# Kernel tuning notes

Hardware: AMD Instinct MI355X
Metric: run time of the kernel (lower is better)

Reference implementation:

```python
import jax, jax.numpy as jnp
import numpy as np

H = 32  # node_hidden_size
B = 16  # number of graphs in the batch


def setup_inputs() -> dict:
    key = jax.random.key(0)
    ks = iter(jax.random.split(key, 32))
    N, E = 20000, 200000
    rn = lambda s, scale=0.1: jax.random.normal(next(ks), s, dtype=jnp.float32) * scale
    return {
        "x": jax.random.normal(next(ks), (N, 4), dtype=jnp.float32),
        "edge_index": jax.random.randint(next(ks), (2, E), 0, N),
        "edge_attr": jax.random.normal(next(ks), (E,), dtype=jnp.float32),
        "batch": jnp.sort(jax.random.randint(next(ks), (N,), 0, B)),
        # project: Linear(4,32)
        "proj_w": rn((4, H)), "proj_b": jnp.zeros((H,), jnp.float32),
        # edge_nn: Linear(1,8) -> ReLU -> Linear(8,32*32)
        "e1_w": rn((1, 8)), "e1_b": jnp.zeros((8,), jnp.float32),
        "e2_w": rn((8, H * H)), "e2_b": jnp.zeros((H * H,), jnp.float32),
        # NNConv root weight + bias
        "root_w": rn((H, H)), "conv_b": jnp.zeros((H,), jnp.float32),
        # GRU(32,32), torch layout [3H, in]/[3H, H], gate order r,z,n
        "gru_wi": rn((3 * H, H)), "gru_wh": rn((3 * H, H)),
        "gru_bi": jnp.zeros((3 * H,), jnp.float32), "gru_bh": jnp.zeros((3 * H,), jnp.float32),
        # Set2Set LSTM(2H -> H), gate order i,f,g,o
        "lstm_wi": rn((4 * H, 2 * H)), "lstm_wh": rn((4 * H, H)),
        "lstm_bi": jnp.zeros((4 * H,), jnp.float32), "lstm_bh": jnp.zeros((4 * H,), jnp.float32),
        # FFN: 2H -> H -> H -> 1 (dropout is identity at inference)
        "f1_w": rn((2 * H, H)), "f1_b": jnp.zeros((H,), jnp.float32),
        "f2_w": rn((H, H)), "f2_b": jnp.zeros((H,), jnp.float32),
        "f3_w": rn((H, 1)), "f3_b": jnp.zeros((1,), jnp.float32),
    }


def reference(x, edge_index, edge_attr, batch,
              proj_w, proj_b, e1_w, e1_b, e2_w, e2_b, root_w, conv_b,
              gru_wi, gru_wh, gru_bi, gru_bh,
              lstm_wi, lstm_wh, lstm_bi, lstm_bh,
              f1_w, f1_b, f2_w, f2_b, f3_w, f3_b):
    N = x.shape[0]
    src, dst = edge_index[0], edge_index[1]

    # project node features
    h = jax.nn.relu(x @ proj_w + proj_b)              # [N, H]
    msg = h                                           # GRU hidden state

    # edge-conditioned weights (edge_attr unsqueezed to [E,1]); constant over steps
    ea = edge_attr[:, None]
    ew = (jax.nn.relu(ea @ e1_w + e1_b) @ e2_w + e2_b).reshape(-1, H, H)  # [E, in, out]

    for _ in range(3):  # message passing steps
        m = jnp.einsum('ei,eio->eo', h[src], ew)                  # per-edge matvec [E, H]
        agg = jax.ops.segment_sum(m, dst, num_segments=N)         # scatter-add to targets
        out = jax.nn.relu(agg + h @ root_w + conv_b)              # NNConv root + bias, then ReLU
        # GRU cell (seq_len=1)
        gi = out @ gru_wi.T + gru_bi
        gh = msg @ gru_wh.T + gru_bh
        r = jax.nn.sigmoid(gi[:, :H] + gh[:, :H])
        z = jax.nn.sigmoid(gi[:, H:2 * H] + gh[:, H:2 * H])
        n = jnp.tanh(gi[:, 2 * H:] + r * gh[:, 2 * H:])
        h = (1.0 - z) * n + z * msg
        msg = h

    # Set2Set readout, processing_steps=1
    q_star = jnp.zeros((B, 2 * H), x.dtype)
    hL = jnp.zeros((B, H), x.dtype)
    cL = jnp.zeros((B, H), x.dtype)
    g = q_star @ lstm_wi.T + lstm_bi + hL @ lstm_wh.T + lstm_bh   # [B, 4H]
    i_g = jax.nn.sigmoid(g[:, :H])
    f_g = jax.nn.sigmoid(g[:, H:2 * H])
    g_g = jnp.tanh(g[:, 2 * H:3 * H])
    o_g = jax.nn.sigmoid(g[:, 3 * H:])
    cL = f_g * cL + i_g * g_g
    q = o_g * jnp.tanh(cL)                                        # [B, H]
    # per-graph softmax attention
    e = jnp.sum(h * q[batch], axis=-1)                            # [N]
    e_max = jax.ops.segment_max(e, batch, num_segments=B)
    a = jnp.exp(e - e_max[batch])
    a = a / jax.ops.segment_sum(a, batch, num_segments=B)[batch]
    r_out = jax.ops.segment_sum(a[:, None] * h, batch, num_segments=B)  # [B, H]
    q_star = jnp.concatenate([q, r_out], axis=-1)                 # [B, 2H]

    # FFN (dropout = identity at inference)
    out = jax.nn.relu(q_star @ f1_w + f1_b)
    out = jax.nn.relu(out @ f2_w + f2_b)
    return out @ f3_w + f3_b                                      # [B, 1]
```

## Files before the change

### kernel.cpp

```cpp
#include <hip/hip_runtime.h>
#include <math.h>

#define H 32
#define BSEG 16
#define CHUNKS 32

#define FMA4(acc, s, wv) { acc[0]=fmaf(s,wv.x,acc[0]); acc[1]=fmaf(s,wv.y,acc[1]); acc[2]=fmaf(s,wv.z,acc[2]); acc[3]=fmaf(s,wv.w,acc[3]); }

__device__ __forceinline__ float sigmoidf_(float x){ return 1.f/(1.f+expf(-x)); }

__device__ __forceinline__ unsigned int fenc(float f) {
    int i = __float_as_int(f);
    return (i >= 0) ? ((unsigned int)i | 0x80000000u) : ~(unsigned int)i;
}
__device__ __forceinline__ float fdec(unsigned int u) {
    int i = (u & 0x80000000u) ? (int)(u & 0x7FFFFFFFu) : (int)(~u);
    return __int_as_float(i);
}

__global__ __launch_bounds__(512) void k_prep(
    const float* __restrict__ gru_wi, const float* __restrict__ gru_wh,
    const float* __restrict__ gru_bi, const float* __restrict__ gru_bh,
    const float* __restrict__ lstm_bi, const float* __restrict__ lstm_bh,
    const float* __restrict__ e1w, const float* __restrict__ e1b, const float* __restrict__ e2w,
    float* __restrict__ WI, float* __restrict__ WH, float* __restrict__ BS,
    float* __restrict__ MP, float* __restrict__ MM, int* __restrict__ flag,
    float* __restrict__ qvec, unsigned int* __restrict__ segmax,
    float* __restrict__ ssum, float* __restrict__ vsum,
    int* __restrict__ cnt, int N)
{
    int t = threadIdx.x;
    for (int i = t; i < N; i += 512) cnt[i] = 0;
    for (int idx = t; idx < 3072; idx += 512) {
        int k = idx >> 10, rem = idx & 1023, i = rem >> 5, o = rem & 31;
        WI[idx] = gru_wi[(k*32 + o)*32 + i];
        WH[idx] = gru_wh[(k*32 + o)*32 + i];
    }
    for (int idx = t; idx < 1024; idx += 512) {
        float mp = 0.f, mm = 0.f;
        #pragma unroll
        for (int k = 0; k < 8; ++k) {
            float w = e1w[k];
            float v = e2w[k*1024 + idx];
            if (w > 0.f) mp = fmaf(w, v, mp);
            if (w < 0.f) mm = fmaf(w, v, mm);
        }
        MP[idx] = mp;
        MM[idx] = mm;
    }
    if (t == 0) {
        int z = 1;
        for (int k = 0; k < 8; ++k) if (e1b[k] != 0.f) z = 0;
        flag[0] = z;
    }
    if (t < 32) {
        BS[t]      = gru_bi[t]      + gru_bh[t];
        BS[32 + t] = gru_bi[32 + t] + gru_bh[32 + t];
        BS[64 + t] = gru_bi[64 + t];
        BS[96 + t] = gru_bh[64 + t];
    }
    if (t < H) {
        float g0 = lstm_bi[t] + lstm_bh[t];
        float g2 = lstm_bi[2*H + t] + lstm_bh[2*H + t];
        float g3 = lstm_bi[3*H + t] + lstm_bh[3*H + t];
        float ig = sigmoidf_(g0);
        float gg = tanhf(g2);
        float og = sigmoidf_(g3);
        qvec[t] = og * tanhf(ig * gg);
    }
    for (int i = t; i < BSEG; i += 512) { segmax[i] = 0u; ssum[i] = 0.f; }
    for (int i = t; i < BSEG*H; i += 512) vsum[i] = 0.f;
}

__global__ __launch_bounds__(256) void k_count(const int* __restrict__ ei, int* __restrict__ cnt, int E)
{
    int e = blockIdx.x * 256 + threadIdx.x;
    if (e < E) atomicAdd(&cnt[ei[E + e]], 1);
}

__global__ __launch_bounds__(1024) void k_scan(
    const int* __restrict__ cnt, int* __restrict__ rowptr, int* __restrict__ cursor, int N)
{
    __shared__ int part[1024];
    int t = threadIdx.x;
    int chunk = (N + 1023) >> 10;
    int base = t * chunk;
    int s = 0;
    for (int i = 0; i < chunk; ++i) {
        int idx = base + i;
        if (idx < N) s += cnt[idx];
    }
    part[t] = s;
    __syncthreads();
    for (int off = 1; off < 1024; off <<= 1) {
        int add = (t >= off) ? part[t - off] : 0;
        __syncthreads();
        part[t] += add;
        __syncthreads();
    }
    int run = part[t] - s;
    for (int i = 0; i < chunk; ++i) {
        int idx = base + i;
        if (idx < N) {
            rowptr[idx] = run;
            cursor[idx] = run;
            run += cnt[idx];
        }
    }
    if (t == 1023) rowptr[N] = part[1023];
}

__global__ __launch_bounds__(256) void k_scatter(
    const int* __restrict__ ei, const float* __restrict__ ea, int* __restrict__ cursor,
    int* __restrict__ esrc, float* __restrict__ eattr, int E)
{
    int e = blockIdx.x * 256 + threadIdx.x;
    if (e >= E) return;
    int dst = ei[E + e];
    int pos = atomicAdd(&cursor[dst], 1);
    esrc[pos] = ei[e];
    eattr[pos] = ea[e];
}

__device__ __forceinline__ void pass2_lds(const float* sm, int xb, int w0, int w1, int fg4,
                                          float a[4], float b[4])
{
    #pragma unroll 2
    for (int i4 = 0; i4 < 32; i4 += 4) {
        float4 xv  = *(const float4*)&sm[xb + i4];
        float4 w00 = *(const float4*)&sm[w0 + (i4+0)*32 + fg4];
        float4 w01 = *(const float4*)&sm[w0 + (i4+1)*32 + fg4];
        float4 w02 = *(const float4*)&sm[w0 + (i4+2)*32 + fg4];
        float4 w03 = *(const float4*)&sm[w0 + (i4+3)*32 + fg4];
        float4 w10 = *(const float4*)&sm[w1 + (i4+0)*32 + fg4];
        float4 w11 = *(const float4*)&sm[w1 + (i4+1)*32 + fg4];
        float4 w12 = *(const float4*)&sm[w1 + (i4+2)*32 + fg4];
        float4 w13 = *(const float4*)&sm[w1 + (i4+3)*32 + fg4];
        FMA4(a, xv.x, w00) FMA4(a, xv.y, w01) FMA4(a, xv.z, w02) FMA4(a, xv.w, w03)
        FMA4(b, xv.x, w10) FMA4(b, xv.y, w11) FMA4(b, xv.z, w12) FMA4(b, xv.w, w13)
    }
}

__device__ __forceinline__ void pass1_lds(const float* sm, int xb, int w0, int fg4, float a[4])
{
    #pragma unroll 2
    for (int i4 = 0; i4 < 32; i4 += 4) {
        float4 xv  = *(const float4*)&sm[xb + i4];
        float4 w00 = *(const float4*)&sm[w0 + (i4+0)*32 + fg4];
        float4 w01 = *(const float4*)&sm[w0 + (i4+1)*32 + fg4];
        float4 w02 = *(const float4*)&sm[w0 + (i4+2)*32 + fg4];
        float4 w03 = *(const float4*)&sm[w0 + (i4+3)*32 + fg4];
        FMA4(a, xv.x, w00) FMA4(a, xv.y, w01) FMA4(a, xv.z, w02) FMA4(a, xv.w, w03)
    }
}

#define TW 3072
__global__ __launch_bounds__(256, 2) void k_tab(
    const float* __restrict__ x, const float* __restrict__ proj_w, const float* __restrict__ proj_b,
    const float* __restrict__ e2w, const float* __restrict__ e2b,
    const float* __restrict__ MP, const float* __restrict__ MM, const int* __restrict__ flag,
    float* __restrict__ h, float* __restrict__ A, int N)
{
    __shared__ float sm[TW + 4*288];
    int tid = threadIdx.x;
    int lane = tid & 63;
    int w = tid >> 6;
    int fg = lane & 7, fg4 = fg*4;
    int nw = lane >> 3;
    int n = (blockIdx.x * 4 + w) * 8 + nw;
    bool valid = (n < N);
    int nc = valid ? n : (N - 1);
    int xb = TW + w*288 + nw*36;

    {
        float4 xv = *(const float4*)&x[nc*4];
        float r_[4];
        #pragma unroll
        for (int j = 0; j < 4; ++j) {
            int o = fg4 + j;
            float a = proj_b[o];
            a = fmaf(xv.x, proj_w[0*32 + o], a);
            a = fmaf(xv.y, proj_w[1*32 + o], a);
            a = fmaf(xv.z, proj_w[2*32 + o], a);
            a = fmaf(xv.w, proj_w[3*32 + o], a);
            r_[j] = fmaxf(a, 0.f);
        }
        if (valid) *(float4*)&h[n*32 + fg4] = make_float4(r_[0], r_[1], r_[2], r_[3]);
        *(float4*)&sm[xb + fg4] = make_float4(r_[0], r_[1], r_[2], r_[3]);
    }

    if (flag[0]) {
        float4* s4 = (float4*)sm;
        for (int i = tid; i < 768; i += 256) {
            const float4* src = (i < 256) ? (const float4*)MP
                              : (i < 512) ? (const float4*)MM
                                          : (const float4*)e2b;
            s4[i] = src[i & 255];
        }
        __syncthreads();
        #pragma unroll 1
        for (int cc = 0; cc < 3; ++cc) {
            float acc[4] = {0.f, 0.f, 0.f, 0.f};
            pass1_lds(sm, xb, cc*1024, fg4, acc);
            if (valid)
                *(float4*)&A[(size_t)n*96 + cc*32 + fg4] =
                    make_float4(acc[0], acc[1], acc[2], acc[3]);
        }
    } else {
        #pragma unroll 1
        for (int cg = 0; cg < 3; ++cg) {
            __syncthreads();
            float4* s4 = (float4*)sm;
            for (int i = tid; i < 768; i += 256) {
                int c = cg*3 + (i >> 8);
                const float4* src = (c < 8) ? (const float4*)(e2w + (size_t)c*1024)
                                            : (const float4*)e2b;
                s4[i] = src[i & 255];
            }
            __syncthreads();
            #pragma unroll 1
            for (int cc = 0; cc < 3; ++cc) {
                float acc[4] = {0.f, 0.f, 0.f, 0.f};
                pass1_lds(sm, xb, cc*1024, fg4, acc);
                if (valid)
                    *(float4*)&A[(size_t)n*288 + (cg*3+cc)*32 + fg4] =
                        make_float4(acc[0], acc[1], acc[2], acc[3]);
            }
        }
    }
}

#define XGR 10240
__global__ __launch_bounds__(256, 2) void k_gru(
    float* __restrict__ h,
    const int* __restrict__ rowptr, const int* __restrict__ esrc, const float* __restrict__ eattr,
    const float* __restrict__ TIN, const int* __restrict__ flag,
    const float* __restrict__ root_w, const float* __restrict__ conv_b,
    const float* __restrict__ WI, const float* __restrict__ WH, const float* __restrict__ BS,
    const float* __restrict__ MP, const float* __restrict__ MM,
    const float* __restrict__ e2b, const float* __restrict__ e2w,
    const float* __restrict__ e1w, const float* __restrict__ e1b,
    float* __restrict__ TOUT, int N, int computeT)
{
    __shared__ float sm[XGR + 1152];
    int tid = threadIdx.x;
    int fast = flag[0];
    {
        float4* s4 = (float4*)sm;
        const float4* r4  = (const float4*)root_w;
        const float4* wh4 = (const float4*)WH;
        const float4* wi4 = (const float4*)WI;
        for (int i = tid; i < 256; i += 256) s4[i] = r4[i];
        for (int i = tid; i < 768; i += 256) s4[256  + i] = wh4[i];
        for (int i = tid; i < 768; i += 256) s4[1024 + i] = wi4[i];
        if (computeT && fast) {
            for (int i = tid; i < 768; i += 256) {
                const float4* src = (i < 256) ? (const float4*)MP
                                  : (i < 512) ? (const float4*)MM
                                              : (const float4*)e2b;
                s4[1792 + i] = src[i & 255];
            }
        }
    }
    __syncthreads();

    int lane = tid & 63;
    int w = tid >> 6;
    int fg = lane & 7, fg4 = fg*4;
    int nw = lane >> 3;
    int n = (blockIdx.x * 4 + w) * 8 + nw;
    bool valid = (n < N);
    int nc = valid ? n : (N - 1);
    int xb = XGR + w*288 + nw*36;

    float4 hv4 = *(const float4*)&h[nc*32 + fg4];
    float hold[4] = {hv4.x, hv4.y, hv4.z, hv4.w};
    *(float4*)&sm[xb + fg4] = hv4;

    float av[4] = {0.f, 0.f, 0.f, 0.f};
    {
        int beg = rowptr[nc];
        int end = rowptr[nc + 1];
        if (fast) {
            int j = beg;
            for (; j + 3 < end; j += 4) {
                int s0 = esrc[j],     s1 = esrc[j + 1];
                int s2 = esrc[j + 2], s3 = esrc[j + 3];
                float a0 = eattr[j],     a1 = eattr[j + 1];
                float a2 = eattr[j + 2], a3 = eattr[j + 3];
                const float* p0 = TIN + (size_t)s0 * 96;
                const float* p1 = TIN + (size_t)s1 * 96;
                const float* p2 = TIN + (size_t)s2 * 96;
                const float* p3 = TIN + (size_t)s3 * 96;
                float4 q0 = *(const float4*)&p0[(a0 > 0.f ? 0 : 32) + fg4];
                float4 r0 = *(const float4*)&p0[64 + fg4];
                float4 q1 = *(const float4*)&p1[(a1 > 0.f ? 0 : 32) + fg4];
                float4 r1 = *(const float4*)&p1[64 + fg4];
                float4 q2 = *(const float4*)&p2[(a2 > 0.f ? 0 : 32) + fg4];
                float4 r2 = *(const float4*)&p2[64 + fg4];
                float4 q3 = *(const float4*)&p3[(a3 > 0.f ? 0 : 32) + fg4];
                float4 r3 = *(const float4*)&p3[64 + fg4];
                av[0] += fmaf(a0, q0.x, r0.x) + fmaf(a1, q1.x, r1.x)
                       + fmaf(a2, q2.x, r2.x) + fmaf(a3, q3.x, r3.x);
                av[1] += fmaf(a0, q0.y, r0.y) + fmaf(a1, q1.y, r1.y)
                       + fmaf(a2, q2.y, r2.y) + fmaf(a3, q3.y, r3.y);
                av[2] += fmaf(a0, q0.z, r0.z) + fmaf(a1, q1.z, r1.z)
                       + fmaf(a2, q2.z, r2.z) + fmaf(a3, q3.z, r3.z);
                av[3] += fmaf(a0, q0.w, r0.w) + fmaf(a1, q1.w, r1.w)
                       + fmaf(a2, q2.w, r2.w) + fmaf(a3, q3.w, r3.w);
            }
            for (; j < end; ++j) {
                int s0 = esrc[j];
                float a0 = eattr[j];
                const float* p0 = TIN + (size_t)s0 * 96;
                float4 q0 = *(const float4*)&p0[(a0 > 0.f ? 0 : 32) + fg4];
                float4 r0 = *(const float4*)&p0[64 + fg4];
                av[0] += fmaf(a0, q0.x, r0.x);
                av[1] += fmaf(a0, q0.y, r0.y);
                av[2] += fmaf(a0, q0.z, r0.z);
                av[3] += fmaf(a0, q0.w, r0.w);
            }
        } else {
            for (int j = beg; j < end; ++j) {
                int src = esrc[j];
                float a = eattr[j];
                const float* Gp = TIN + (size_t)src * 288;
                float4 b = *(const float4*)&Gp[256 + fg4];
                float m0 = b.x, m1 = b.y, m2 = b.z, m3 = b.w;
                #pragma unroll
                for (int k = 0; k < 8; ++k) {
                    float t = fmaxf(fmaf(a, e1w[k], e1b[k]), 0.f);
                    float4 g = *(const float4*)&Gp[k*32 + fg4];
                    m0 = fmaf(t, g.x, m0); m1 = fmaf(t, g.y, m1);
                    m2 = fmaf(t, g.z, m2); m3 = fmaf(t, g.w, m3);
                }
                av[0] += m0; av[1] += m1; av[2] += m2; av[3] += m3;
            }
        }
    }

    float outv[4], gh2[4];
    {
        float4 cb4 = *(const float4*)&conv_b[fg4];
        outv[0]=av[0]+cb4.x; outv[1]=av[1]+cb4.y; outv[2]=av[2]+cb4.z; outv[3]=av[3]+cb4.w;
        float4 b3 = *(const float4*)&BS[96 + fg4];
        gh2[0]=b3.x; gh2[1]=b3.y; gh2[2]=b3.z; gh2[3]=b3.w;
    }
    pass2_lds(sm, xb, 0, 1024 + 2048, fg4, outv, gh2);

    float gh0[4] = {0.f,0.f,0.f,0.f};
    float gh1[4] = {0.f,0.f,0.f,0.f};
    pass2_lds(sm, xb, 1024, 2048, fg4, gh0, gh1);

    float outr[4];
    #pragma unroll
    for (int j = 0; j < 4; ++j) outr[j] = fmaxf(outv[j], 0.f);

    *(float4*)&sm[xb + fg4] = make_float4(outr[0], outr[1], outr[2], outr[3]);

    float gi0[4], gi1[4], gi2[4];
    {
        float4 b0 = *(const float4*)&BS[fg4];
        float4 b1 = *(const float4*)&BS[32 + fg4];
        float4 b2 = *(const float4*)&BS[64 + fg4];
        gi0[0]=b0.x; gi0[1]=b0.y; gi0[2]=b0.z; gi0[3]=b0.w;
        gi1[0]=b1.x; gi1[1]=b1.y; gi1[2]=b1.z; gi1[3]=b1.w;
        gi2[0]=b2.x; gi2[1]=b2.y; gi2[2]=b2.z; gi2[3]=b2.w;
    }
    pass2_lds(sm, xb, 4096, 5120, fg4, gi0, gi1);
    pass1_lds(sm, xb, 6144, fg4, gi2);

    float hnew[4];
    #pragma unroll
    for (int j = 0; j < 4; ++j) {
        float r = sigmoidf_(gi0[j] + gh0[j]);
        float z = sigmoidf_(gi1[j] + gh1[j]);
        float nn = tanhf(gi2[j] + r * gh2[j]);
        hnew[j] = (1.f - z) * nn + z * hold[j];
    }
    if (valid) *(float4*)&h[n*32 + fg4] = make_float4(hnew[0], hnew[1], hnew[2], hnew[3]);

    if (computeT) {
        *(float4*)&sm[xb + fg4] = make_float4(hnew[0], hnew[1], hnew[2], hnew[3]);
        if (fast) {
            #pragma unroll 1
            for (int cc = 0; cc < 3; ++cc) {
                float acc[4] = {0.f, 0.f, 0.f, 0.f};
                pass1_lds(sm, xb, 7168 + cc*1024, fg4, acc);
                if (valid)
                    *(float4*)&TOUT[(size_t)n*96 + cc*32 + fg4] =
                        make_float4(acc[0], acc[1], acc[2], acc[3]);
            }
        } else {
            #pragma unroll 1
            for (int cg = 0; cg < 3; ++cg) {
                __syncthreads();
                float4* s4 = (float4*)sm;
                for (int i = tid; i < 768; i += 256) {
                    int c = cg*3 + (i >> 8);
                    const float4* src = (c < 8) ? (const float4*)(e2w + (size_t)c*1024)
                                                : (const float4*)e2b;
                    s4[1792 + i] = src[i & 255];
                }
                __syncthreads();
                #pragma unroll 1
                for (int cc = 0; cc < 3; ++cc) {
                    float acc[4] = {0.f, 0.f, 0.f, 0.f};
                    pass1_lds(sm, xb, 7168 + cc*1024, fg4, acc);
                    if (valid)
                        *(float4*)&TOUT[(size_t)n*288 + (cg*3+cc)*32 + fg4] =
                            make_float4(acc[0], acc[1], acc[2], acc[3]);
                }
            }
        }
    }
}

__global__ __launch_bounds__(256) void k_pass1(
    const float* __restrict__ h, const int* __restrict__ batch,
    const float* __restrict__ qvec, float* __restrict__ ebuf,
    unsigned int* __restrict__ segmax, int N)
{
    int b = blockIdx.x / CHUNKS;
    int c = blockIdx.x % CHUNKS;
    int lo = 0, hi = N;
    while (lo < hi) { int mid = (lo + hi) >> 1; if (batch[mid] < b) lo = mid + 1; else hi = mid; }
    int s = lo;
    lo = 0; hi = N;
    while (lo < hi) { int mid = (lo + hi) >> 1; if (batch[mid] < b + 1) lo = mid + 1; else hi = mid; }
    int e = lo;
    int len = e - s;
    int per = (len + CHUNKS - 1) / CHUNKS;
    int n0 = s + c * per;
    int n1 = min(n0 + per, e);

    int tid = threadIdx.x;
    int ln = tid >> 5, o = tid & 31;
    float qv = qvec[o];
    float mloc = -INFINITY;
    for (int nn = n0 + ln; nn < n1; nn += 8) {
        float v = h[nn * H + o] * qv;
        #pragma unroll
        for (int m = 16; m >= 1; m >>= 1) v += __shfl_xor(v, m);
        if (o == 0) ebuf[nn] = v;
        mloc = fmaxf(mloc, v);
    }
    __shared__ float red[256];
    red[tid] = mloc;
    __syncthreads();
    for (int st = 128; st >= 1; st >>= 1) {
        if (tid < st) red[tid] = fmaxf(red[tid], red[tid + st]);
        __syncthreads();
    }
    if (tid == 0 && n0 < n1) atomicMax(&segmax[b], fenc(red[0]));
}

__global__ __launch_bounds__(256) void k_pass2(
    const float* __restrict__ h, const int* __restrict__ batch,
    const float* __restrict__ ebuf, const unsigned int* __restrict__ segmax,
    float* __restrict__ ssum, float* __restrict__ vsum, int N)
{
    int b = blockIdx.x / CHUNKS;
    int c = blockIdx.x % CHUNKS;
    int lo = 0, hi = N;
    while (lo < hi) { int mid = (lo + hi) >> 1; if (batch[mid] < b) lo = mid + 1; else hi = mid; }
    int s = lo;
    lo = 0; hi = N;
    while (lo < hi) { int mid = (lo + hi) >> 1; if (batch[mid] < b + 1) lo = mid + 1; else hi = mid; }
    int e = lo;
    int len = e - s;
    int per = (len + CHUNKS - 1) / CHUNKS;
    int n0 = s + c * per;
    int n1 = min(n0 + per, e);

    int tid = threadIdx.x;
    int ln = tid >> 5, o = tid & 31;
    float emax = fdec(segmax[b]);
    float vacc = 0.f, sacc = 0.f;
    for (int nn = n0 + ln; nn < n1; nn += 8) {
        float a = expf(ebuf[nn] - emax);
        vacc += a * h[nn * H + o];
        if (o == 0) sacc += a;
    }
    __shared__ float vsh[8][H];
    __shared__ float ssh[8];
    vsh[ln][o] = vacc;
    if (o == 0) ssh[ln] = sacc;
    __syncthreads();
    if (tid < H) {
        float v = 0.f;
        #pragma unroll
        for (int g = 0; g < 8; ++g) v += vsh[g][tid];
        atomicAdd(&vsum[b * H + tid], v);
    } else if (tid == H) {
        float stot = 0.f;
        #pragma unroll
        for (int g = 0; g < 8; ++g) stot += ssh[g];
        atomicAdd(&ssum[b], stot);
    }
}

__global__ __launch_bounds__(512) void k_mlp(
    const float* __restrict__ qvec, const float* __restrict__ ssum, const float* __restrict__ vsum,
    const float* __restrict__ f1w, const float* __restrict__ f1b,
    const float* __restrict__ f2w, const float* __restrict__ f2b,
    const float* __restrict__ f3w, const float* __restrict__ f3b,
    float* __restrict__ out)
{
    __shared__ float qsm[BSEG][2 * H];
    __shared__ float o1[BSEG][H];
    __shared__ float o2[BSEG][H];
    int tid = threadIdx.x;
    int b = tid >> 5, j = tid & 31;
    float st = ssum[b];
    qsm[b][j] = qvec[j];
    qsm[b][H + j] = (st > 0.f) ? vsum[b * H + j] / st : 0.f;
    __syncthreads();
    float acc = f1b[j];
    for (int i = 0; i < 2 * H; ++i) acc += qsm[b][i] * f1w[i * H + j];
    o1[b][j] = fmaxf(acc, 0.f);
    __syncthreads();
    acc = f2b[j];
    for (int i = 0; i < H; ++i) acc += o1[b][i] * f2w[i * H + j];
    o2[b][j] = fmaxf(acc, 0.f);
    __syncthreads();
    float v = o2[b][j] * f3w[j];
    #pragma unroll
    for (int m = 16; m >= 1; m >>= 1) v += __shfl_xor(v, m);
    if (j == 0) out[b] = v + f3b[0];
}

extern "C" void kernel_launch(void* const* d_in, const int* in_sizes, int n_in,
                              void* d_out, int out_size, void* d_ws, size_t ws_size,
                              hipStream_t stream)
{
    const float* x      = (const float*)d_in[0];
    const int*   ei     = (const int*)d_in[1];
    const float* ea     = (const float*)d_in[2];
    const int*   batch  = (const int*)d_in[3];
    const float* proj_w = (const float*)d_in[4];
    const float* proj_b = (const float*)d_in[5];
    const float* e1w    = (const float*)d_in[6];
    const float* e1b    = (const float*)d_in[7];
    const float* e2w    = (const float*)d_in[8];
    const float* e2b    = (const float*)d_in[9];
    const float* root_w = (const float*)d_in[10];
    const float* conv_b = (const float*)d_in[11];
    const float* gru_wi = (const float*)d_in[12];
    const float* gru_wh = (const float*)d_in[13];
    const float* gru_bi = (const float*)d_in[14];
    const float* gru_bh = (const float*)d_in[15];
    const float* lstm_bi = (const float*)d_in[18];
    const float* lstm_bh = (const float*)d_in[19];
    const float* f1w    = (const float*)d_in[20];
    const float* f1b    = (const float*)d_in[21];
    const float* f2w    = (const float*)d_in[22];
    const float* f2b    = (const float*)d_in[23];
    const float* f3w    = (const float*)d_in[24];
    const float* f3b    = (const float*)d_in[25];

    const int N = in_sizes[0] / 4;
    const int E = in_sizes[2];

    float* ws   = (float*)d_ws;
    float* h    = ws;
    float* A    = h + (size_t)N * H;
    float* Bb   = A + (size_t)N * 288;
    float* ebuf = Bb + (size_t)N * 288;
    float* qvec = ebuf + N;
    unsigned int* segmax = (unsigned int*)(qvec + H);
    float* ssum = (float*)(segmax + BSEG);
    float* vsum = ssum + BSEG;
    float* WI   = vsum + BSEG * H;
    float* WH   = WI + 3072;
    float* BS   = WH + 3072;
    float* MP   = BS + 128;
    float* MM   = MP + 1024;
    int*   flag = (int*)(MM + 1024);
    int*   cnt    = flag + 1;
    int*   rowptr = cnt + N;
    int*   cursor = rowptr + N + 1;
    int*   esrc   = cursor + N;
    float* eattr  = (float*)(esrc + E);

    const int nwaves = (N + 7) / 8;
    const int nb4 = (nwaves + 3) / 4;
    const int cblocks = (E + 255) / 256;

    k_prep<<<1, 512, 0, stream>>>(gru_wi, gru_wh, gru_bi, gru_bh, lstm_bi, lstm_bh,
                                  e1w, e1b, e2w,
                                  WI, WH, BS, MP, MM, flag, qvec, segmax, ssum, vsum, cnt, N);
    k_count<<<cblocks, 256, 0, stream>>>(ei, cnt, E);
    k_scan<<<1, 1024, 0, stream>>>(cnt, rowptr, cursor, N);
    k_scatter<<<cblocks, 256, 0, stream>>>(ei, ea, cursor, esrc, eattr, E);
    k_tab<<<nb4, 256, 0, stream>>>(x, proj_w, proj_b, e2w, e2b, MP, MM, flag, h, A, N);

    k_gru<<<nb4, 256, 0, stream>>>(h, rowptr, esrc, eattr, A, flag, root_w, conv_b,
                                   WI, WH, BS, MP, MM, e2b, e2w, e1w, e1b, Bb, N, 1);
    k_gru<<<nb4, 256, 0, stream>>>(h, rowptr, esrc, eattr, Bb, flag, root_w, conv_b,
                                   WI, WH, BS, MP, MM, e2b, e2w, e1w, e1b, A, N, 1);
    k_gru<<<nb4, 256, 0, stream>>>(h, rowptr, esrc, eattr, A, flag, root_w, conv_b,
                                   WI, WH, BS, MP, MM, e2b, e2w, e1w, e1b, Bb, N, 0);

    k_pass1<<<BSEG * CHUNKS, 256, 0, stream>>>(h, batch, qvec, ebuf, segmax, N);
    k_pass2<<<BSEG * CHUNKS, 256, 0, stream>>>(h, batch, ebuf, segmax, ssum, vsum, N);
    k_mlp<<<1, 512, 0, stream>>>(qvec, ssum, vsum, f1w, f1b, f2w, f2b, f3w, f3b, (float*)d_out);
}
```

Before: 181.9 us.

## Aggregate raw neighbor features then apply edge weight matrices once per node

```diff
diff --git a/kernel.cpp b/kernel.cpp
--- a/kernel.cpp
+++ b/kernel.cpp
@@ -158,7 +158,7 @@
 __global__ __launch_bounds__(256, 2) void k_tab(
     const float* __restrict__ x, const float* __restrict__ proj_w, const float* __restrict__ proj_b,
     const float* __restrict__ e2w, const float* __restrict__ e2b,
-    const float* __restrict__ MP, const float* __restrict__ MM, const int* __restrict__ flag,
+    const int* __restrict__ flag,
     float* __restrict__ h, float* __restrict__ A, int N)
 {
     __shared__ float sm[TW + 4*288];
@@ -189,24 +189,7 @@
         *(float4*)&sm[xb + fg4] = make_float4(r_[0], r_[1], r_[2], r_[3]);
     }
 
-    if (flag[0]) {
-        float4* s4 = (float4*)sm;
-        for (int i = tid; i < 768; i += 256) {
-            const float4* src = (i < 256) ? (const float4*)MP
-                              : (i < 512) ? (const float4*)MM
-                                          : (const float4*)e2b;
-            s4[i] = src[i & 255];
-        }
-        __syncthreads();
-        #pragma unroll 1
-        for (int cc = 0; cc < 3; ++cc) {
-            float acc[4] = {0.f, 0.f, 0.f, 0.f};
-            pass1_lds(sm, xb, cc*1024, fg4, acc);
-            if (valid)
-                *(float4*)&A[(size_t)n*96 + cc*32 + fg4] =
-                    make_float4(acc[0], acc[1], acc[2], acc[3]);
-        }
-    } else {
+    if (!flag[0]) {
         #pragma unroll 1
         for (int cg = 0; cg < 3; ++cg) {
             __syncthreads();
@@ -232,7 +215,7 @@
 
 #define XGR 10240
 __global__ __launch_bounds__(256, 2) void k_gru(
-    float* __restrict__ h,
+    const float* __restrict__ hIN, float* __restrict__ hOUT,
     const int* __restrict__ rowptr, const int* __restrict__ esrc, const float* __restrict__ eattr,
     const float* __restrict__ TIN, const int* __restrict__ flag,
     const float* __restrict__ root_w, const float* __restrict__ conv_b,
@@ -253,7 +236,7 @@
         for (int i = tid; i < 256; i += 256) s4[i] = r4[i];
         for (int i = tid; i < 768; i += 256) s4[256  + i] = wh4[i];
         for (int i = tid; i < 768; i += 256) s4[1024 + i] = wi4[i];
-        if (computeT && fast) {
+        if (fast) {
             for (int i = tid; i < 768; i += 256) {
                 const float4* src = (i < 256) ? (const float4*)MP
                                   : (i < 512) ? (const float4*)MM
@@ -273,72 +256,73 @@
     int nc = valid ? n : (N - 1);
     int xb = XGR + w*288 + nw*36;
 
-    float4 hv4 = *(const float4*)&h[nc*32 + fg4];
+    float4 hv4 = *(const float4*)&hIN[nc*32 + fg4];
     float hold[4] = {hv4.x, hv4.y, hv4.z, hv4.w};
-    *(float4*)&sm[xb + fg4] = hv4;
 
     float av[4] = {0.f, 0.f, 0.f, 0.f};
-    {
+    if (fast) {
+        float up[4] = {0.f,0.f,0.f,0.f};
+        float um[4] = {0.f,0.f,0.f,0.f};
+        float u0[4] = {0.f,0.f,0.f,0.f};
         int beg = rowptr[nc];
         int end = rowptr[nc + 1];
-        if (fast) {
-            int j = beg;
-            for (; j + 3 < end; j += 4) {
-                int s0 = esrc[j],     s1 = esrc[j + 1];
-                int s2 = esrc[j + 2], s3 = esrc[j + 3];
-                float a0 = eattr[j],     a1 = eattr[j + 1];
-                float a2 = eattr[j + 2], a3 = eattr[j + 3];
-                const float* p0 = TIN + (size_t)s0 * 96;
-                const float* p1 = TIN + (size_t)s1 * 96;
-                const float* p2 = TIN + (size_t)s2 * 96;
-                const float* p3 = TIN + (size_t)s3 * 96;
-                float4 q0 = *(const float4*)&p0[(a0 > 0.f ? 0 : 32) + fg4];
-                float4 r0 = *(const float4*)&p0[64 + fg4];
-                float4 q1 = *(const float4*)&p1[(a1 > 0.f ? 0 : 32) + fg4];
-                float4 r1 = *(const float4*)&p1[64 + fg4];
-                float4 q2 = *(const float4*)&p2[(a2 > 0.f ? 0 : 32) + fg4];
-                float4 r2 = *(const float4*)&p2[64 + fg4];
-                float4 q3 = *(const float4*)&p3[(a3 > 0.f ? 0 : 32) + fg4];
-                float4 r3 = *(const float4*)&p3[64 + fg4];
-                av[0] += fmaf(a0, q0.x, r0.x) + fmaf(a1, q1.x, r1.x)
-                       + fmaf(a2, q2.x, r2.x) + fmaf(a3, q3.x, r3.x);
-                av[1] += fmaf(a0, q0.y, r0.y) + fmaf(a1, q1.y, r1.y)
-                       + fmaf(a2, q2.y, r2.y) + fmaf(a3, q3.y, r3.y);
-                av[2] += fmaf(a0, q0.z, r0.z) + fmaf(a1, q1.z, r1.z)
-                       + fmaf(a2, q2.z, r2.z) + fmaf(a3, q3.z, r3.z);
-                av[3] += fmaf(a0, q0.w, r0.w) + fmaf(a1, q1.w, r1.w)
-                       + fmaf(a2, q2.w, r2.w) + fmaf(a3, q3.w, r3.w);
+        int j = beg;
+        for (; j + 3 < end; j += 4) {
+            int s0 = esrc[j],     s1 = esrc[j + 1];
+            int s2 = esrc[j + 2], s3 = esrc[j + 3];
+            float a0 = eattr[j],     a1 = eattr[j + 1];
+            float a2 = eattr[j + 2], a3 = eattr[j + 3];
+            float4 g0 = *(const float4*)&hIN[(size_t)s0*32 + fg4];
+            float4 g1 = *(const float4*)&hIN[(size_t)s1*32 + fg4];
+            float4 g2 = *(const float4*)&hIN[(size_t)s2*32 + fg4];
+            float4 g3 = *(const float4*)&hIN[(size_t)s3*32 + fg4];
+            float p0 = fmaxf(a0, 0.f), m0 = fminf(a0, 0.f);
+            float p1 = fmaxf(a1, 0.f), m1 = fminf(a1, 0.f);
+            float p2 = fmaxf(a2, 0.f), m2 = fminf(a2, 0.f);
+            float p3 = fmaxf(a3, 0.f), m3 = fminf(a3, 0.f);
+            FMA4(up, p0, g0) FMA4(up, p1, g1) FMA4(up, p2, g2) FMA4(up, p3, g3)
+            FMA4(um, m0, g0) FMA4(um, m1, g1) FMA4(um, m2, g2) FMA4(um, m3, g3)
+            u0[0] += g0.x + g1.x + g2.x + g3.x;
+            u0[1] += g0.y + g1.y + g2.y + g3.y;
+            u0[2] += g0.z + g1.z + g2.z + g3.z;
+            u0[3] += g0.w + g1.w + g2.w + g3.w;
+        }
+        for (; j < end; ++j) {
+            int s0 = esrc[j];
+            float a0 = eattr[j];
+            float4 g0 = *(const float4*)&hIN[(size_t)s0*32 + fg4];
+            float p0 = fmaxf(a0, 0.f), m0 = fminf(a0, 0.f);
+            FMA4(up, p0, g0)
+            FMA4(um, m0, g0)
+            u0[0] += g0.x; u0[1] += g0.y; u0[2] += g0.z; u0[3] += g0.w;
+        }
+        *(float4*)&sm[xb + fg4] = make_float4(up[0], up[1], up[2], up[3]);
+        pass1_lds(sm, xb, 7168, fg4, av);
+        *(float4*)&sm[xb + fg4] = make_float4(um[0], um[1], um[2], um[3]);
+        pass1_lds(sm, xb, 8192, fg4, av);
+        *(float4*)&sm[xb + fg4] = make_float4(u0[0], u0[1], u0[2], u0[3]);
+        pass1_lds(sm, xb, 9216, fg4, av);
+    } else {
+        int beg = rowptr[nc];
+        int end = rowptr[nc + 1];
+        for (int j = beg; j < end; ++j) {
+            int src = esrc[j];
+            float a = eattr[j];
+            const float* Gp = TIN + (size_t)src * 288;
+            float4 b = *(const float4*)&Gp[256 + fg4];
+            float m0 = b.x, m1 = b.y, m2 = b.z, m3 = b.w;
+            #pragma unroll
+            for (int k = 0; k < 8; ++k) {
+                float t = fmaxf(fmaf(a, e1w[k], e1b[k]), 0.f);
+                float4 g = *(const float4*)&Gp[k*32 + fg4];
+                m0 = fmaf(t, g.x, m0); m1 = fmaf(t, g.y, m1);
+                m2 = fmaf(t, g.z, m2); m3 = fmaf(t, g.w, m3);
             }
-            for (; j < end; ++j) {
-                int s0 = esrc[j];
-                float a0 = eattr[j];
-                const float* p0 = TIN + (size_t)s0 * 96;
-                float4 q0 = *(const float4*)&p0[(a0 > 0.f ? 0 : 32) + fg4];
-                float4 r0 = *(const float4*)&p0[64 + fg4];
-                av[0] += fmaf(a0, q0.x, r0.x);
-                av[1] += fmaf(a0, q0.y, r0.y);
-                av[2] += fmaf(a0, q0.z, r0.z);
-                av[3] += fmaf(a0, q0.w, r0.w);
-            }
-        } else {
-            for (int j = beg; j < end; ++j) {
-                int src = esrc[j];
-                float a = eattr[j];
-                const float* Gp = TIN + (size_t)src * 288;
-                float4 b = *(const float4*)&Gp[256 + fg4];
-                float m0 = b.x, m1 = b.y, m2 = b.z, m3 = b.w;
-                #pragma unroll
-                for (int k = 0; k < 8; ++k) {
-                    float t = fmaxf(fmaf(a, e1w[k], e1b[k]), 0.f);
-                    float4 g = *(const float4*)&Gp[k*32 + fg4];
-                    m0 = fmaf(t, g.x, m0); m1 = fmaf(t, g.y, m1);
-                    m2 = fmaf(t, g.z, m2); m3 = fmaf(t, g.w, m3);
-                }
-                av[0] += m0; av[1] += m1; av[2] += m2; av[3] += m3;
-            }
-        }
-    }
-
+            av[0] += m0; av[1] += m1; av[2] += m2; av[3] += m3;
+        }
+    }
+
+    *(float4*)&sm[xb + fg4] = hv4;
     float outv[4], gh2[4];
     {
         float4 cb4 = *(const float4*)&conv_b[fg4];
@@ -378,39 +362,28 @@
         float nn = tanhf(gi2[j] + r * gh2[j]);
         hnew[j] = (1.f - z) * nn + z * hold[j];
     }
-    if (valid) *(float4*)&h[n*32 + fg4] = make_float4(hnew[0], hnew[1], hnew[2], hnew[3]);
-
-    if (computeT) {
+    if (valid) *(float4*)&hOUT[n*32 + fg4] = make_float4(hnew[0], hnew[1], hnew[2], hnew[3]);
+
+    if (!fast && computeT) {
         *(float4*)&sm[xb + fg4] = make_float4(hnew[0], hnew[1], hnew[2], hnew[3]);
-        if (fast) {
+        #pragma unroll 1
+        for (int cg = 0; cg < 3; ++cg) {
+            __syncthreads();
+            float4* s4 = (float4*)sm;
+            for (int i = tid; i < 768; i += 256) {
+                int c = cg*3 + (i >> 8);
+                const float4* src = (c < 8) ? (const float4*)(e2w + (size_t)c*1024)
+                                            : (const float4*)e2b;
+                s4[1792 + i] = src[i & 255];
+            }
+            __syncthreads();
             #pragma unroll 1
             for (int cc = 0; cc < 3; ++cc) {
                 float acc[4] = {0.f, 0.f, 0.f, 0.f};
                 pass1_lds(sm, xb, 7168 + cc*1024, fg4, acc);
                 if (valid)
-                    *(float4*)&TOUT[(size_t)n*96 + cc*32 + fg4] =
+                    *(float4*)&TOUT[(size_t)n*288 + (cg*3+cc)*32 + fg4] =
                         make_float4(acc[0], acc[1], acc[2], acc[3]);
-            }
-        } else {
-            #pragma unroll 1
-            for (int cg = 0; cg < 3; ++cg) {
-                __syncthreads();
-                float4* s4 = (float4*)sm;
-                for (int i = tid; i < 768; i += 256) {
-                    int c = cg*3 + (i >> 8);
-                    const float4* src = (c < 8) ? (const float4*)(e2w + (size_t)c*1024)
-                                                : (const float4*)e2b;
-                    s4[1792 + i] = src[i & 255];
-                }
-                __syncthreads();
-                #pragma unroll 1
-                for (int cc = 0; cc < 3; ++cc) {
-                    float acc[4] = {0.f, 0.f, 0.f, 0.f};
-                    pass1_lds(sm, xb, 7168 + cc*1024, fg4, acc);
-                    if (valid)
-                        *(float4*)&TOUT[(size_t)n*288 + (cg*3+cc)*32 + fg4] =
-                            make_float4(acc[0], acc[1], acc[2], acc[3]);
-                }
             }
         }
     }
@@ -563,8 +536,9 @@
     const int E = in_sizes[2];
 
     float* ws   = (float*)d_ws;
-    float* h    = ws;
-    float* A    = h + (size_t)N * H;
+    float* hA   = ws;
+    float* hB   = hA + (size_t)N * H;
+    float* A    = hB + (size_t)N * H;
     float* Bb   = A + (size_t)N * 288;
     float* ebuf = Bb + (size_t)N * 288;
     float* qvec = ebuf + N;
@@ -593,16 +567,16 @@
     k_count<<<cblocks, 256, 0, stream>>>(ei, cnt, E);
     k_scan<<<1, 1024, 0, stream>>>(cnt, rowptr, cursor, N);
     k_scatter<<<cblocks, 256, 0, stream>>>(ei, ea, cursor, esrc, eattr, E);
-    k_tab<<<nb4, 256, 0, stream>>>(x, proj_w, proj_b, e2w, e2b, MP, MM, flag, h, A, N);
-
-    k_gru<<<nb4, 256, 0, stream>>>(h, rowptr, esrc, eattr, A, flag, root_w, conv_b,
+    k_tab<<<nb4, 256, 0, stream>>>(x, proj_w, proj_b, e2w, e2b, flag, hA, A, N);
+
+    k_gru<<<nb4, 256, 0, stream>>>(hA, hB, rowptr, esrc, eattr, A, flag, root_w, conv_b,
                                    WI, WH, BS, MP, MM, e2b, e2w, e1w, e1b, Bb, N, 1);
-    k_gru<<<nb4, 256, 0, stream>>>(h, rowptr, esrc, eattr, Bb, flag, root_w, conv_b,
+    k_gru<<<nb4, 256, 0, stream>>>(hB, hA, rowptr, esrc, eattr, Bb, flag, root_w, conv_b,
                                    WI, WH, BS, MP, MM, e2b, e2w, e1w, e1b, A, N, 1);
-    k_gru<<<nb4, 256, 0, stream>>>(h, rowptr, esrc, eattr, A, flag, root_w, conv_b,
+    k_gru<<<nb4, 256, 0, stream>>>(hA, hB, rowptr, esrc, eattr, A, flag, root_w, conv_b,
                                    WI, WH, BS, MP, MM, e2b, e2w, e1w, e1b, Bb, N, 0);
 
-    k_pass1<<<BSEG * CHUNKS, 256, 0, stream>>>(h, batch, qvec, ebuf, segmax, N);
-    k_pass2<<<BSEG * CHUNKS, 256, 0, stream>>>(h, batch, ebuf, segmax, ssum, vsum, N);
+    k_pass1<<<BSEG * CHUNKS, 256, 0, stream>>>(hB, batch, qvec, ebuf, segmax, N);
+    k_pass2<<<BSEG * CHUNKS, 256, 0, stream>>>(hB, batch, ebuf, segmax, ssum, vsum, N);
     k_mlp<<<1, 512, 0, stream>>>(qvec, ssum, vsum, f1w, f1b, f2w, f2b, f3w, f3b, (float*)d_out);
 }
```

Measured after the change: 167.7 us (median of 2 runs). -7.8%, faster.
